# Performance work log

Measured on AMD Instinct MI355X. Metric: run time of the kernel, lower is better.

Reference implementation:

```python
import jax, jax.numpy as jnp
import numpy as np

N = 100000      # nodes
E = 1000000     # edges (nnz of adj)
DIN = 128
DOUT = 64
MAX_W = 0.05    # max_weight in project_column_stochastic


def setup_inputs() -> dict:
    key = jax.random.key(0)
    k1, k2, k3, k4 = jax.random.split(key, 4)
    x = jax.random.normal(k1, (N, DIN), dtype=jnp.float32)
    edge_index = jax.random.randint(k2, (2, E), 0, N)  # [2, E] (row, col) of sparse adj
    edge_vals = jax.random.uniform(k3, (E,), dtype=jnp.float32)
    # column-stochastic init, mirroring reset_parameters():
    # uniform(0,1) -> clamp(min=threshold=0, max=0.05) -> column normalize
    w = jax.random.uniform(k4, (DIN, DOUT), dtype=jnp.float32)
    w = jnp.clip(w, 0.0, MAX_W)
    w = w / jnp.clip(w.sum(axis=0, keepdims=True), 1e-8, None)
    bias = jnp.zeros((DOUT,), dtype=jnp.float32)
    return {"input": x, "edge_index": edge_index, "edge_vals": edge_vals,
            "weight": w, "bias": bias}


def reference(input, edge_index, edge_vals, weight, bias):
    # support = input @ weight  (dense projection)
    support = input @ weight                          # [N, DOUT]
    # output = spmm(adj, support): gather source rows, scale by nnz value,
    # scatter-add into destination rows.
    rows, cols = edge_index[0], edge_index[1]
    msgs = edge_vals[:, None] * support[cols]         # [E, DOUT]
    out = jax.ops.segment_sum(msgs, rows, num_segments=input.shape[0])  # [N, DOUT]
    return out + bias
```

## Files before the change

kernel.cpp:

```cpp
#include <hip/hip_runtime.h>
#include <hip/hip_bf16.h>

#define DIN 128
#define DOUT 64
#define BROWS 256
#define MAXBKT 512
#define NGEMM 391
#define NHIST 64
#define PART_BLOCK 512
#define PART_VPT 8
#define PART_CHUNK (PART_BLOCK * PART_VPT)
#define CAP 3584
#define ACC_VPT 4
#define WSTRIDE 136

typedef short short8 __attribute__((ext_vector_type(8)));
typedef float f32x4 __attribute__((ext_vector_type(4)));

union U4S8 { uint4 u; short8 s; };
union BF2U { __hip_bfloat162 h; unsigned int u; };

__device__ inline unsigned int f2bf(float f) {
    union { float f; unsigned int u; } v; v.f = f;
    unsigned int u = v.u;
    u += 0x7fffu + ((u >> 16) & 1u);
    return u >> 16;
}

__global__ __launch_bounds__(512) void gemm_hist_kernel(const float* __restrict__ x,
                                                        const float* __restrict__ w,
                                                        unsigned short* __restrict__ support,
                                                        int ntiles,
                                                        const int* __restrict__ rows,
                                                        int* __restrict__ cnt,
                                                        int* __restrict__ base,
                                                        int* __restrict__ cursor,
                                                        int* __restrict__ done,
                                                        int E, int nb) {
    int tid = threadIdx.x;
    if (blockIdx.x < NGEMM) {
        __shared__ unsigned short wlds[DOUT * WSTRIDE];
        for (int i = tid; i < DIN * DOUT; i += 512) {
            int k = i >> 6, n = i & 63;
            wlds[n * WSTRIDE + k] = (unsigned short)f2bf(w[i]);
        }
        __syncthreads();

        int lane = tid & 63, quad = lane >> 4, mlo = lane & 15;
        U4S8 wf[16];
#pragma unroll
        for (int kt = 0; kt < 4; ++kt)
#pragma unroll
            for (int nt = 0; nt < 4; ++nt)
                wf[kt * 4 + nt].u = *((const uint4*)(wlds + (nt * 16 + mlo) * WSTRIDE + kt * 32 + quad * 8));

        int wave0 = (blockIdx.x * 512 + tid) >> 6;
        int nwaves = NGEMM * 8;

        for (int tile = wave0; tile < ntiles; tile += nwaves) {
            const float4* p = (const float4*)(x + ((size_t)tile * 16 + mlo) * DIN + quad * 8);
            float4 fv[8];
#pragma unroll
            for (int kt = 0; kt < 4; ++kt) {
                fv[2 * kt]     = p[kt * 8];
                fv[2 * kt + 1] = p[kt * 8 + 1];
            }
            U4S8 af[4];
#pragma unroll
            for (int kt = 0; kt < 4; ++kt) {
                float4 a = fv[2 * kt], b = fv[2 * kt + 1];
                BF2U u0, u1, u2, u3;
                u0.h = __float22bfloat162_rn(make_float2(a.x, a.y));
                u1.h = __float22bfloat162_rn(make_float2(a.z, a.w));
                u2.h = __float22bfloat162_rn(make_float2(b.x, b.y));
                u3.h = __float22bfloat162_rn(make_float2(b.z, b.w));
                uint4 u; u.x = u0.u; u.y = u1.u; u.z = u2.u; u.w = u3.u;
                af[kt].u = u;
            }

            f32x4 acc[4] = {};
#pragma unroll
            for (int nt = 0; nt < 4; ++nt)
#pragma unroll
                for (int kt = 0; kt < 4; ++kt)
                    acc[nt] = __builtin_amdgcn_mfma_f32_16x16x32_bf16(af[kt].s, wf[kt * 4 + nt].s, acc[nt], 0, 0, 0);

#pragma unroll
            for (int nt = 0; nt < 4; ++nt)
#pragma unroll
                for (int r = 0; r < 4; ++r)
                    support[((size_t)tile * 16 + quad * 4 + r) * DOUT + nt * 16 + mlo] =
                        (unsigned short)f2bf(acc[nt][r]);
        }
    } else {
        __shared__ int c[MAXBKT];
        __shared__ int ticket;
        c[tid] = 0;
        __syncthreads();
        int bh = blockIdx.x - NGEMM;
        for (int e = bh * 512 + tid; e < E; e += NHIST * 512)
            atomicAdd(&c[rows[e] >> 8], 1);
        __syncthreads();
        int v = c[tid];
        if (v) atomicAdd(&cnt[tid], v);
        __syncthreads();
        __threadfence();
        if (tid == 0) ticket = atomicAdd(done, 1);
        __syncthreads();
        if (ticket != NHIST - 1) return;
        if (tid >= 64) return;
        int lane = tid;
        int run = 0;
        for (int i0 = 0; i0 < nb; i0 += 64) {
            int cv = (i0 + lane < nb)
                         ? __hip_atomic_load(&cnt[i0 + lane], __ATOMIC_RELAXED, __HIP_MEMORY_SCOPE_AGENT)
                         : 0;
            int incl = cv;
            for (int o = 1; o < 64; o <<= 1) {
                int t = __shfl_up(incl, o);
                if (lane >= o) incl += t;
            }
            if (i0 + lane < nb) {
                base[i0 + lane]   = run + incl - cv;
                cursor[i0 + lane] = run + incl - cv;
            }
            run += __shfl(incl, 63);
        }
        if (lane == 0) base[nb] = run;
    }
}

__global__ __launch_bounds__(PART_BLOCK) void partition_kernel(const int* __restrict__ rows,
                                                               const int* __restrict__ cols,
                                                               const float* __restrict__ vals,
                                                               int* __restrict__ bucket_cursor,
                                                               uint2* __restrict__ tmp, int E) {
    __shared__ int cnt[MAXBKT];
    __shared__ int off[MAXBKT];
    __shared__ int gbase[MAXBKT];
    __shared__ int wsum[PART_BLOCK / 64];
    __shared__ int lkey[PART_CHUNK];
    __shared__ int lval[PART_CHUNK];
    __shared__ short lbkt[PART_CHUNK];

    int tid = threadIdx.x;
    int base = blockIdx.x * PART_CHUNK;

    cnt[tid] = 0;
    __syncthreads();

    int myr[PART_VPT], myc[PART_VPT], myrank[PART_VPT];
    float myv[PART_VPT];
#pragma unroll
    for (int i = 0; i < PART_VPT; ++i) {
        int e = base + i * PART_BLOCK + tid;
        if (e < E) {
            myr[i] = rows[e];
            myc[i] = cols[e];
            myv[i] = vals[e];
            myrank[i] = atomicAdd(&cnt[myr[i] >> 8], 1);
        }
    }
    __syncthreads();

    int c0 = cnt[tid];
    int lane = tid & 63, wid = tid >> 6;
    int ts = c0;
    for (int o = 1; o < 64; o <<= 1) {
        int t = __shfl_up(ts, o);
        if (lane >= o) ts += t;
    }
    if (lane == 63) wsum[wid] = ts;
    __syncthreads();
    int wb = 0;
    for (int w = 0; w < wid; ++w) wb += wsum[w];
    off[tid] = wb + ts - c0;
    if (c0 > 0) gbase[tid] = atomicAdd(&bucket_cursor[tid], c0);
    __syncthreads();

    int total = off[MAXBKT - 1] + cnt[MAXBKT - 1];

#pragma unroll
    for (int i = 0; i < PART_VPT; ++i) {
        int e = base + i * PART_BLOCK + tid;
        if (e < E) {
            int b = myr[i] >> 8;
            int pos = off[b] + myrank[i];
            lkey[pos] = ((myr[i] & (BROWS - 1)) << 17) | myc[i];
            lval[pos] = __float_as_int(myv[i]);
            lbkt[pos] = (short)b;
        }
    }
    __syncthreads();

    for (int s = tid; s < total; s += PART_BLOCK) {
        int b = lbkt[s];
        int d = gbase[b] + (s - off[b]);
        tmp[d] = make_uint2((unsigned)lkey[s], (unsigned)lval[s]);
    }
}

__global__ __launch_bounds__(1024) void accum_kernel(const int* __restrict__ bucket_base,
                                                     const uint2* __restrict__ tmp,
                                                     const unsigned short* __restrict__ support,
                                                     const float* __restrict__ bias,
                                                     float* __restrict__ out, int N) {
    __shared__ int cnt[BROWS];
    __shared__ int rstart[BROWS];
    __shared__ int cur[BROWS];
    __shared__ int wsum4[4];
    __shared__ uint2 list[CAP];

    int b = blockIdx.x;
    int rbase = b * BROWS;
    int nrows = min(BROWS, N - rbase);
    int tid = threadIdx.x, lane = tid & 63, wv = tid >> 6;
    int start = bucket_base[b], end = bucket_base[b + 1];

    if (tid < BROWS) cnt[tid] = 0;
    __syncthreads();

    uint2 kv[ACC_VPT];
#pragma unroll
    for (int i = 0; i < ACC_VPT; ++i) {
        int s = start + i * 1024 + tid;
        if (s < end) {
            kv[i] = tmp[s];
            atomicAdd(&cnt[kv[i].x >> 17], 1);
        }
    }
    for (int s = start + ACC_VPT * 1024 + tid; s < end; s += 1024)
        atomicAdd(&cnt[tmp[s].x >> 17], 1);
    __syncthreads();

    int v = 0, incl = 0;
    if (tid < BROWS) {
        v = cnt[tid]; incl = v;
        for (int o = 1; o < 64; o <<= 1) {
            int t = __shfl_up(incl, o);
            if (lane >= o) incl += t;
        }
        if (lane == 63) wsum4[wv] = incl;
    }
    __syncthreads();
    if (tid < BROWS) {
        int wb = 0;
        for (int w = 0; w < wv; ++w) wb += wsum4[w];
        int st = wb + incl - v;
        rstart[tid] = st;
        cur[tid] = st;
    }
    __syncthreads();

#pragma unroll
    for (int i = 0; i < ACC_VPT; ++i) {
        int s = start + i * 1024 + tid;
        if (s < end) {
            int p = atomicAdd(&cur[kv[i].x >> 17], 1);
            if (p < CAP) list[p] = kv[i];
        }
    }
    for (int s = start + ACC_VPT * 1024 + tid; s < end; s += 1024) {
        uint2 k2 = tmp[s];
        int p = atomicAdd(&cur[k2.x >> 17], 1);
        if (p < CAP) list[p] = k2;
    }
    __syncthreads();

    int half = lane >> 5, cl = lane & 31;
    float2 bl = ((const float2*)bias)[cl];
    for (int rp = wv * 2 + half; rp < nrows; rp += 32) {
        int s = min(rstart[rp], CAP);
        int e2 = min(s + cnt[rp], CAP);
        float a0 = 0.f, a1 = 0.f, c0 = 0.f, c1 = 0.f;
        for (; s + 4 <= e2; s += 4) {
            uint2 ea = list[s], eb = list[s + 1], ec = list[s + 2], ed = list[s + 3];
            unsigned ga = *((const unsigned*)(support + (size_t)(ea.x & 0x1FFFF) * DOUT) + cl);
            unsigned gb = *((const unsigned*)(support + (size_t)(eb.x & 0x1FFFF) * DOUT) + cl);
            unsigned gc = *((const unsigned*)(support + (size_t)(ec.x & 0x1FFFF) * DOUT) + cl);
            unsigned gd = *((const unsigned*)(support + (size_t)(ed.x & 0x1FFFF) * DOUT) + cl);
            float va = __uint_as_float(ea.y), vb = __uint_as_float(eb.y);
            float vc = __uint_as_float(ec.y), vd = __uint_as_float(ed.y);
            a0 = fmaf(va, __uint_as_float(ga << 16), a0);
            a1 = fmaf(va, __uint_as_float(ga & 0xffff0000u), a1);
            c0 = fmaf(vb, __uint_as_float(gb << 16), c0);
            c1 = fmaf(vb, __uint_as_float(gb & 0xffff0000u), c1);
            a0 = fmaf(vc, __uint_as_float(gc << 16), a0);
            a1 = fmaf(vc, __uint_as_float(gc & 0xffff0000u), a1);
            c0 = fmaf(vd, __uint_as_float(gd << 16), c0);
            c1 = fmaf(vd, __uint_as_float(gd & 0xffff0000u), c1);
        }
        for (; s < e2; ++s) {
            uint2 ea = list[s];
            unsigned ga = *((const unsigned*)(support + (size_t)(ea.x & 0x1FFFF) * DOUT) + cl);
            float va = __uint_as_float(ea.y);
            a0 = fmaf(va, __uint_as_float(ga << 16), a0);
            a1 = fmaf(va, __uint_as_float(ga & 0xffff0000u), a1);
        }
        float2 o;
        o.x = a0 + c0 + bl.x;
        o.y = a1 + c1 + bl.y;
        *((float2*)(out + (size_t)(rbase + rp) * DOUT) + cl) = o;
    }
}

extern "C" void kernel_launch(void* const* d_in, const int* in_sizes, int n_in,
                              void* d_out, int out_size, void* d_ws, size_t ws_size,
                              hipStream_t stream) {
    const float* x    = (const float*)d_in[0];
    const int*   ei   = (const int*)d_in[1];
    const float* ev   = (const float*)d_in[2];
    const float* w    = (const float*)d_in[3];
    const float* bias = (const float*)d_in[4];
    float* out = (float*)d_out;

    const int N = in_sizes[0] / DIN;
    const int E = in_sizes[2];
    const int* rows = ei;
    const int* cols = ei + E;
    const int nbuckets = (N + BROWS - 1) / BROWS;

    char* ws = (char*)d_ws;
    size_t off = 0;
    auto take = [&](size_t bytes) { char* p = ws + off; off = (off + bytes + 255) & ~(size_t)255; return p; };
    unsigned short* support       = (unsigned short*)take((size_t)N * DOUT * sizeof(unsigned short));
    int*            bucket_cnt    = (int*)take((MAXBKT + 1) * sizeof(int));
    int*            bucket_base   = (int*)take((MAXBKT + 1) * sizeof(int));
    int*            bucket_cursor = (int*)take(MAXBKT * sizeof(int));
    uint2*          tmp           = (uint2*)take((size_t)E * sizeof(uint2));
    (void)ws_size;
    int* done = bucket_cnt + MAXBKT;

    hipMemsetAsync(bucket_cnt, 0, (MAXBKT + 1) * sizeof(int), stream);

    int ntiles = N / 16;
    gemm_hist_kernel<<<NGEMM + NHIST, 512, 0, stream>>>(x, w, support, ntiles,
                                                        rows, bucket_cnt, bucket_base,
                                                        bucket_cursor, done, E, nbuckets);

    partition_kernel<<<(E + PART_CHUNK - 1) / PART_CHUNK, PART_BLOCK, 0, stream>>>(
        rows, cols, ev, bucket_cursor, tmp, E);

    accum_kernel<<<nbuckets, 1024, 0, stream>>>(bucket_base, tmp, support, bias, out, N);
}
```

Before: 167.0 us.

## Fuse partition into GEMM kernel using fixed-capacity buckets, drop histogram pass

Removes the separate histogram/prefix-scan stage and merges edge partitioning into the GEMM launch so both run concurrently. Buckets now use fixed CAP-sized slots indexed by atomic cursors, and accumulation reads the cursor as the bucket length. This saves a kernel launch and a pass over row indices. In exchange, edges past CAP in a bucket are dropped, which is correct only when no bucket overflows.

```diff
diff --git a/kernel.cpp b/kernel.cpp
--- a/kernel.cpp
+++ b/kernel.cpp
@@ -6,7 +6,6 @@
 #define BROWS 256
 #define MAXBKT 512
 #define NGEMM 391
-#define NHIST 64
 #define PART_BLOCK 512
 #define PART_VPT 8
 #define PART_CHUNK (PART_BLOCK * PART_VPT)
@@ -27,19 +26,36 @@
     return u >> 16;
 }
 
-__global__ __launch_bounds__(512) void gemm_hist_kernel(const float* __restrict__ x,
+struct PartSmem {
+    int cnt[MAXBKT];
+    int off[MAXBKT];
+    int gbase[MAXBKT];
+    int wsum[PART_BLOCK / 64];
+    int lkey[PART_CHUNK];
+    int lval[PART_CHUNK];
+    short lbkt[PART_CHUNK];
+};
+struct GemmSmem {
+    unsigned short wlds[DOUT * WSTRIDE];
+};
+union FusedSmem {
+    PartSmem p;
+    GemmSmem g;
+};
+
+__global__ __launch_bounds__(512) void gemm_part_kernel(const float* __restrict__ x,
                                                         const float* __restrict__ w,
                                                         unsigned short* __restrict__ support,
                                                         int ntiles,
                                                         const int* __restrict__ rows,
-                                                        int* __restrict__ cnt,
-                                                        int* __restrict__ base,
-                                                        int* __restrict__ cursor,
-                                                        int* __restrict__ done,
-                                                        int E, int nb) {
+                                                        const int* __restrict__ cols,
+                                                        const float* __restrict__ vals,
+                                                        int* __restrict__ bucket_cursor,
+                                                        uint2* __restrict__ tmp, int E) {
+    __shared__ FusedSmem sm;
     int tid = threadIdx.x;
     if (blockIdx.x < NGEMM) {
-        __shared__ unsigned short wlds[DOUT * WSTRIDE];
+        unsigned short* wlds = sm.g.wlds;
         for (int i = tid; i < DIN * DOUT; i += 512) {
             int k = i >> 6, n = i & 63;
             wlds[n * WSTRIDE + k] = (unsigned short)f2bf(w[i]);
@@ -93,114 +109,73 @@
                         (unsigned short)f2bf(acc[nt][r]);
         }
     } else {
-        __shared__ int c[MAXBKT];
-        __shared__ int ticket;
-        c[tid] = 0;
-        __syncthreads();
-        int bh = blockIdx.x - NGEMM;
-        for (int e = bh * 512 + tid; e < E; e += NHIST * 512)
-            atomicAdd(&c[rows[e] >> 8], 1);
-        __syncthreads();
-        int v = c[tid];
-        if (v) atomicAdd(&cnt[tid], v);
-        __syncthreads();
-        __threadfence();
-        if (tid == 0) ticket = atomicAdd(done, 1);
-        __syncthreads();
-        if (ticket != NHIST - 1) return;
-        if (tid >= 64) return;
-        int lane = tid;
-        int run = 0;
-        for (int i0 = 0; i0 < nb; i0 += 64) {
-            int cv = (i0 + lane < nb)
-                         ? __hip_atomic_load(&cnt[i0 + lane], __ATOMIC_RELAXED, __HIP_MEMORY_SCOPE_AGENT)
-                         : 0;
-            int incl = cv;
-            for (int o = 1; o < 64; o <<= 1) {
-                int t = __shfl_up(incl, o);
-                if (lane >= o) incl += t;
+        int* cnt   = sm.p.cnt;
+        int* off   = sm.p.off;
+        int* gbase = sm.p.gbase;
+        int* wsum  = sm.p.wsum;
+        int* lkey  = sm.p.lkey;
+        int* lval  = sm.p.lval;
+        short* lbkt = sm.p.lbkt;
+
+        int base = (blockIdx.x - NGEMM) * PART_CHUNK;
+
+        cnt[tid] = 0;
+        __syncthreads();
+
+        int myr[PART_VPT], myc[PART_VPT], myrank[PART_VPT];
+        float myv[PART_VPT];
+#pragma unroll
+        for (int i = 0; i < PART_VPT; ++i) {
+            int e = base + i * PART_BLOCK + tid;
+            if (e < E) {
+                myr[i] = rows[e];
+                myc[i] = cols[e];
+                myv[i] = vals[e];
+                myrank[i] = atomicAdd(&cnt[myr[i] >> 8], 1);
             }
-            if (i0 + lane < nb) {
-                base[i0 + lane]   = run + incl - cv;
-                cursor[i0 + lane] = run + incl - cv;
+        }
+        __syncthreads();
+
+        int c0 = cnt[tid];
+        int lane = tid & 63, wid = tid >> 6;
+        int ts = c0;
+        for (int o = 1; o < 64; o <<= 1) {
+            int t = __shfl_up(ts, o);
+            if (lane >= o) ts += t;
+        }
+        if (lane == 63) wsum[wid] = ts;
+        __syncthreads();
+        int wb = 0;
+        for (int w2 = 0; w2 < wid; ++w2) wb += wsum[w2];
+        off[tid] = wb + ts - c0;
+        if (c0 > 0) gbase[tid] = atomicAdd(&bucket_cursor[tid], c0);
+        __syncthreads();
+
+        int total = off[MAXBKT - 1] + cnt[MAXBKT - 1];
+
+#pragma unroll
+        for (int i = 0; i < PART_VPT; ++i) {
+            int e = base + i * PART_BLOCK + tid;
+            if (e < E) {
+                int b = myr[i] >> 8;
+                int pos = off[b] + myrank[i];
+                lkey[pos] = ((myr[i] & (BROWS - 1)) << 17) | myc[i];
+                lval[pos] = __float_as_int(myv[i]);
+                lbkt[pos] = (short)b;
             }
-            run += __shfl(incl, 63);
-        }
-        if (lane == 0) base[nb] = run;
+        }
+        __syncthreads();
+
+        for (int s = tid; s < total; s += PART_BLOCK) {
+            int b = lbkt[s];
+            int pos = gbase[b] + (s - off[b]);
+            if (pos < CAP)
+                tmp[(size_t)b * CAP + pos] = make_uint2((unsigned)lkey[s], (unsigned)lval[s]);
+        }
     }
 }
 
-__global__ __launch_bounds__(PART_BLOCK) void partition_kernel(const int* __restrict__ rows,
-                                                               const int* __restrict__ cols,
-                                                               const float* __restrict__ vals,
-                                                               int* __restrict__ bucket_cursor,
-                                                               uint2* __restrict__ tmp, int E) {
-    __shared__ int cnt[MAXBKT];
-    __shared__ int off[MAXBKT];
-    __shared__ int gbase[MAXBKT];
-    __shared__ int wsum[PART_BLOCK / 64];
-    __shared__ int lkey[PART_CHUNK];
-    __shared__ int lval[PART_CHUNK];
-    __shared__ short lbkt[PART_CHUNK];
-
-    int tid = threadIdx.x;
-    int base = blockIdx.x * PART_CHUNK;
-
-    cnt[tid] = 0;
-    __syncthreads();
-
-    int myr[PART_VPT], myc[PART_VPT], myrank[PART_VPT];
-    float myv[PART_VPT];
-#pragma unroll
-    for (int i = 0; i < PART_VPT; ++i) {
-        int e = base + i * PART_BLOCK + tid;
-        if (e < E) {
-            myr[i] = rows[e];
-            myc[i] = cols[e];
-            myv[i] = vals[e];
-            myrank[i] = atomicAdd(&cnt[myr[i] >> 8], 1);
-        }
-    }
-    __syncthreads();
-
-    int c0 = cnt[tid];
-    int lane = tid & 63, wid = tid >> 6;
-    int ts = c0;
-    for (int o = 1; o < 64; o <<= 1) {
-        int t = __shfl_up(ts, o);
-        if (lane >= o) ts += t;
-    }
-    if (lane == 63) wsum[wid] = ts;
-    __syncthreads();
-    int wb = 0;
-    for (int w = 0; w < wid; ++w) wb += wsum[w];
-    off[tid] = wb + ts - c0;
-    if (c0 > 0) gbase[tid] = atomicAdd(&bucket_cursor[tid], c0);
-    __syncthreads();
-
-    int total = off[MAXBKT - 1] + cnt[MAXBKT - 1];
-
-#pragma unroll
-    for (int i = 0; i < PART_VPT; ++i) {
-        int e = base + i * PART_BLOCK + tid;
-        if (e < E) {
-            int b = myr[i] >> 8;
-            int pos = off[b] + myrank[i];
-            lkey[pos] = ((myr[i] & (BROWS - 1)) << 17) | myc[i];
-            lval[pos] = __float_as_int(myv[i]);
-            lbkt[pos] = (short)b;
-        }
-    }
-    __syncthreads();
-
-    for (int s = tid; s < total; s += PART_BLOCK) {
-        int b = lbkt[s];
-        int d = gbase[b] + (s - off[b]);
-        tmp[d] = make_uint2((unsigned)lkey[s], (unsigned)lval[s]);
-    }
-}
-
-__global__ __launch_bounds__(1024) void accum_kernel(const int* __restrict__ bucket_base,
+__global__ __launch_bounds__(1024) void accum_kernel(const int* __restrict__ bucket_cursor,
                                                      const uint2* __restrict__ tmp,
                                                      const unsigned short* __restrict__ support,
                                                      const float* __restrict__ bias,
@@ -215,7 +190,8 @@
     int rbase = b * BROWS;
     int nrows = min(BROWS, N - rbase);
     int tid = threadIdx.x, lane = tid & 63, wv = tid >> 6;
-    int start = bucket_base[b], end = bucket_base[b + 1];
+    int start = b * CAP;
+    int end = start + min(bucket_cursor[b], CAP);
 
     if (tid < BROWS) cnt[tid] = 0;
     __syncthreads();
@@ -324,22 +300,17 @@
     size_t off = 0;
     auto take = [&](size_t bytes) { char* p = ws + off; off = (off + bytes + 255) & ~(size_t)255; return p; };
     unsigned short* support       = (unsigned short*)take((size_t)N * DOUT * sizeof(unsigned short));
-    int*            bucket_cnt    = (int*)take((MAXBKT + 1) * sizeof(int));
-    int*            bucket_base   = (int*)take((MAXBKT + 1) * sizeof(int));
     int*            bucket_cursor = (int*)take(MAXBKT * sizeof(int));
-    uint2*          tmp           = (uint2*)take((size_t)E * sizeof(uint2));
+    uint2*          tmp           = (uint2*)take((size_t)nbuckets * CAP * sizeof(uint2));
     (void)ws_size;
-    int* done = bucket_cnt + MAXBKT;
-
-    hipMemsetAsync(bucket_cnt, 0, (MAXBKT + 1) * sizeof(int), stream);
+
+    hipMemsetAsync(bucket_cursor, 0, MAXBKT * sizeof(int), stream);
 
     int ntiles = N / 16;
-    gemm_hist_kernel<<<NGEMM + NHIST, 512, 0, stream>>>(x, w, support, ntiles,
-                                                        rows, bucket_cnt, bucket_base,
-                                                        bucket_cursor, done, E, nbuckets);
-
-    partition_kernel<<<(E + PART_CHUNK - 1) / PART_CHUNK, PART_BLOCK, 0, stream>>>(
-        rows, cols, ev, bucket_cursor, tmp, E);
-
-    accum_kernel<<<nbuckets, 1024, 0, stream>>>(bucket_base, tmp, support, bias, out, N);
+    int npart = (E + PART_CHUNK - 1) / PART_CHUNK;
+    gemm_part_kernel<<<NGEMM + npart, 512, 0, stream>>>(x, w, support, ntiles,
+                                                        rows, cols, ev,
+                                                        bucket_cursor, tmp, E);
+
+    accum_kernel<<<nbuckets, 1024, 0, stream>>>(bucket_cursor, tmp, support, bias, out, N);
 }
```

Result: faster. 140.7 us (-15.7%).
